# Performance work log

Hardware: AMD Instinct MI355X
Metric: run time of the kernel (lower is better)

## Reference

```python
import jax, jax.numpy as jnp
import numpy as np

D_MODEL = 1024
NUM_HEADS = 16
D_K = D_MODEL // NUM_HEADS


def setup_inputs() -> dict:
    key = jax.random.key(0)
    ks = jax.random.split(key, 9)
    B, S = 2, 2048
    scale = 1.0 / np.sqrt(D_MODEL)
    x = jax.random.normal(ks[0], (B, S, D_MODEL), dtype=jnp.float32)
    Wq = jax.random.normal(ks[1], (D_MODEL, D_MODEL), dtype=jnp.float32) * scale
    Wk = jax.random.normal(ks[2], (D_MODEL, D_MODEL), dtype=jnp.float32) * scale
    Wv = jax.random.normal(ks[3], (D_MODEL, D_MODEL), dtype=jnp.float32) * scale
    Wo = jax.random.normal(ks[4], (D_MODEL, D_MODEL), dtype=jnp.float32) * scale
    bq = jax.random.normal(ks[5], (D_MODEL,), dtype=jnp.float32) * 0.01
    bk = jax.random.normal(ks[6], (D_MODEL,), dtype=jnp.float32) * 0.01
    bv = jax.random.normal(ks[7], (D_MODEL,), dtype=jnp.float32) * 0.01
    bo = jax.random.normal(ks[8], (D_MODEL,), dtype=jnp.float32) * 0.01
    return {"x": x, "Wq": Wq, "bq": bq, "Wk": Wk, "bk": bk,
            "Wv": Wv, "bv": bv, "Wo": Wo, "bo": bo}


def reference(x, Wq, bq, Wk, bk, Wv, bv, Wo, bo):
    B, S, _ = x.shape
    H, Dk = NUM_HEADS, D_K
    # projections -> [B, H, S, Dk]
    def split_heads(t):
        return t.reshape(B, S, H, Dk).transpose(0, 2, 1, 3)
    q = split_heads(x @ Wq + bq)
    k = split_heads(x @ Wk + bk)
    v = split_heads(x @ Wv + bv)
    # full score matrix [B, H, S, S] (faithful to the original non-fused impl)
    scores = jnp.einsum('bhqd,bhkd->bhqk', q, k) / jnp.sqrt(jnp.float32(Dk))
    attn = jax.nn.softmax(scores, axis=-1)
    out = jnp.einsum('bhqk,bhkd->bhqd', attn, v)
    out = out.transpose(0, 2, 1, 3).reshape(B, S, H * Dk)
    return out @ Wo + bo
```

## Files before the change

### kernel.cpp

```cpp
#include <hip/hip_runtime.h>
#include <cstdint>

constexpr int S    = 2048;
constexpr int D    = 1024;
constexpr int NH   = 16;
constexpr int DK   = 64;
constexpr int MTOK = 2 * S;

typedef __bf16 bf16x8 __attribute__((ext_vector_type(8)));
typedef __bf16 bf16x4 __attribute__((ext_vector_type(4)));
typedef float  floatx4 __attribute__((ext_vector_type(4)));

__device__ __forceinline__ void async_cp16(const void* g, void* l) {
    __builtin_amdgcn_global_load_lds(
        (const __attribute__((address_space(1))) uint32_t*)g,
        (__attribute__((address_space(3))) uint32_t*)l, 16, 0, 0);
}

__global__ __launch_bounds__(256) void cvt_prep(
    const float* __restrict__ x, __bf16* __restrict__ xb,
    const float* __restrict__ W0, const float* __restrict__ W1,
    const float* __restrict__ W2, const float* __restrict__ W3,
    __bf16* __restrict__ T0, __bf16* __restrict__ T1,
    __bf16* __restrict__ T2, __bf16* __restrict__ T3)
{
    const int t = threadIdx.x;
    if (blockIdx.z == 4) {
        int blk = blockIdx.y * 16 + blockIdx.x;
        const float4* src = (const float4*)x;
        #pragma unroll
        for (int ii = 0; ii < 16; ++ii) {
            int idx = blk * 4096 + ii * 256 + t;
            float4 v = src[idx];
            bf16x4 o;
            o[0] = (__bf16)v.x; o[1] = (__bf16)v.y; o[2] = (__bf16)v.z; o[3] = (__bf16)v.w;
            *(bf16x4*)&xb[(size_t)idx * 4] = o;
        }
        return;
    }
    const float* W = (blockIdx.z == 0) ? W0 : (blockIdx.z == 1) ? W1 : (blockIdx.z == 2) ? W2 : W3;
    __bf16*      T = (blockIdx.z == 0) ? T0 : (blockIdx.z == 1) ? T1 : (blockIdx.z == 2) ? T2 : T3;
    __shared__ __bf16 tile[64][65];
    const int k0 = blockIdx.y * 64, n0 = blockIdx.x * 64;
    #pragma unroll
    for (int i = 0; i < 4; ++i) {
        int k = (t >> 4) + i * 16;
        int n = (t & 15) * 4;
        float4 v = *(const float4*)&W[(size_t)(k0 + k) * D + n0 + n];
        tile[n + 0][k] = (__bf16)v.x;
        tile[n + 1][k] = (__bf16)v.y;
        tile[n + 2][k] = (__bf16)v.z;
        tile[n + 3][k] = (__bf16)v.w;
    }
    __syncthreads();
    #pragma unroll
    for (int i = 0; i < 4; ++i) {
        int n = (t >> 4) + i * 16;
        int k = (t & 15) * 4;
        bf16x4 o;
        o[0] = tile[n][k]; o[1] = tile[n][k + 1]; o[2] = tile[n][k + 2]; o[3] = tile[n][k + 3];
        *(bf16x4*)&T[(size_t)(n0 + n) * D + k0 + k] = o;
    }
}

constexpr int BM = 128, BK = 64;

template<int JT>
__device__ __forceinline__ void gemm_core(
    const __bf16* __restrict__ A, const __bf16* __restrict__ Bt,
    __bf16* Alds, __bf16* Blds, int m0, int n0, floatx4 (&acc)[4][JT])
{
    const int tid = threadIdx.x;
    const int w = tid >> 6, l = tid & 63;
    const int wm = (w >> 1) * 64, wn = (w & 1) * 16 * JT;
    const int lr = l & 15, lg = l >> 4;

    #pragma unroll
    for (int i = 0; i < 4; ++i)
        #pragma unroll
        for (int j = 0; j < JT; ++j)
            acc[i][j] = (floatx4){0.f, 0.f, 0.f, 0.f};

    for (int k0 = 0; k0 < D; k0 += BK) {
        #pragma unroll
        for (int i = 0; i < 4; ++i) {
            int c = i * 256 + tid, row = c >> 3, g = c & 7;
            async_cp16(&A[(size_t)(m0 + row) * D + k0 + g * 8], &Alds[c * 8]);
        }
        #pragma unroll
        for (int i = 0; i < JT; ++i) {
            int c = i * 256 + tid, row = c >> 3, g = c & 7;
            async_cp16(&Bt[(size_t)(n0 + row) * D + k0 + g * 8], &Blds[c * 8]);
        }
        __syncthreads();
        #pragma unroll
        for (int kk = 0; kk < 2; ++kk) {
            bf16x8 af[4], bfr[JT];
            #pragma unroll
            for (int i = 0; i < 4; ++i)
                af[i] = *(const bf16x8*)&Alds[(wm + i * 16 + lr) * BK + kk * 32 + lg * 8];
            #pragma unroll
            for (int j = 0; j < JT; ++j)
                bfr[j] = *(const bf16x8*)&Blds[(wn + j * 16 + lr) * BK + kk * 32 + lg * 8];
            #pragma unroll
            for (int i = 0; i < 4; ++i)
                #pragma unroll
                for (int j = 0; j < JT; ++j)
                    acc[i][j] = __builtin_amdgcn_mfma_f32_16x16x32_bf16(af[i], bfr[j], acc[i][j], 0, 0, 0);
        }
        __syncthreads();
    }
}

__global__ __launch_bounds__(256, 2) void gemm_qkv(
    const __bf16* __restrict__ xb,
    const __bf16* __restrict__ WqT, const __bf16* __restrict__ WkT, const __bf16* __restrict__ WvT,
    const float* __restrict__ bq, const float* __restrict__ bk, const float* __restrict__ bv,
    __bf16* __restrict__ Qb, __bf16* __restrict__ Kb, __bf16* __restrict__ Vt)
{
    __shared__ __align__(16) __bf16 Alds[BM * BK];
    __shared__ __align__(16) __bf16 Blds[128 * BK];
    const int z = blockIdx.z;
    const __bf16* Bt   = (z == 0) ? WqT : (z == 1) ? WkT : WvT;
    const float*  bias = (z == 0) ? bq : (z == 1) ? bk : bv;
    const float   scale = (z == 0) ? 0.18033688f : 1.0f;
    const int m0 = blockIdx.y * BM, n0 = blockIdx.x * 128;

    floatx4 acc[4][4];
    gemm_core<4>(xb, Bt, Alds, Blds, m0, n0, acc);

    const int tid = threadIdx.x;
    const int w = tid >> 6, l = tid & 63;
    const int wm = (w >> 1) * 64, wn = (w & 1) * 64;
    const int lr = l & 15, lg = l >> 4;

    if (z < 2) {
        __bf16* Out = (z == 0) ? Qb : Kb;
        #pragma unroll
        for (int i = 0; i < 4; ++i)
            #pragma unroll
            for (int j = 0; j < 4; ++j) {
                int n = n0 + wn + j * 16 + lr;
                #pragma unroll
                for (int r = 0; r < 4; ++r) {
                    int m = m0 + wm + i * 16 + lg * 4 + r;
                    float v = (acc[i][j][r] + bias[n]) * scale;
                    size_t off = ((size_t)((m >> 11) * NH + (n >> 6)) * S + (m & (S - 1))) * DK + (n & (DK - 1));
                    Out[off] = (__bf16)v;
                }
            }
    } else {
        #pragma unroll
        for (int i = 0; i < 4; ++i)
            #pragma unroll
            for (int j = 0; j < 4; ++j) {
                int n = n0 + wn + j * 16 + lr;
                int m = m0 + wm + i * 16 + lg * 4;
                float bn = bias[n];
                bf16x4 o;
                #pragma unroll
                for (int r = 0; r < 4; ++r) o[r] = (__bf16)(acc[i][j][r] + bn);
                size_t off = ((size_t)((m >> 11) * NH + (n >> 6)) * DK + (n & (DK - 1))) * S + (m & (S - 1));
                *(bf16x4*)&Vt[off] = o;
            }
    }
}

__global__ __launch_bounds__(256, 2) void gemm_out(
    const __bf16* __restrict__ A, const __bf16* __restrict__ Bt,
    const float* __restrict__ bias, float* __restrict__ Cout)
{
    __shared__ __align__(16) __bf16 Alds[BM * BK];
    __shared__ __align__(16) __bf16 Blds[64 * BK];
    const int m0 = blockIdx.y * BM, n0 = blockIdx.x * 64;

    floatx4 acc[4][2];
    gemm_core<2>(A, Bt, Alds, Blds, m0, n0, acc);

    const int tid = threadIdx.x;
    const int w = tid >> 6, l = tid & 63;
    const int wm = (w >> 1) * 64, wn = (w & 1) * 32;
    const int lr = l & 15, lg = l >> 4;
    #pragma unroll
    for (int i = 0; i < 4; ++i)
        #pragma unroll
        for (int j = 0; j < 2; ++j) {
            int n = n0 + wn + j * 16 + lr;
            #pragma unroll
            for (int r = 0; r < 4; ++r) {
                int m = m0 + wm + i * 16 + lg * 4 + r;
                Cout[(size_t)m * D + n] = acc[i][j][r] + bias[n];
            }
        }
}

constexpr int QT = 128;
constexpr int KT = 64;
constexpr float SOFTMAX_C2 = 14.4269504f;

__global__ __launch_bounds__(256, 2) void attn_mfma(
    const __bf16* __restrict__ Q, const __bf16* __restrict__ K,
    const __bf16* __restrict__ Vt, __bf16* __restrict__ O)
{
    __shared__ __align__(16) __bf16 Klds[2][KT * DK];
    __shared__ __align__(16) __bf16 Vlds[2][DK * KT];
    __shared__ __align__(16) __bf16 Plds[4][32 * 64];

    const int tid = threadIdx.x;
    const int w = tid >> 6, l = tid & 63;
    const int lr = l & 15, lg = l >> 4;
    const int sw = lr & 7;
    const int bh = blockIdx.y;
    const int q0 = blockIdx.x * QT;
    const __bf16* Kbase = K  + (size_t)bh * S * DK;
    const __bf16* Vbase = Vt + (size_t)bh * DK * S;

    bf16x8 qf[2][2];
    {
        const __bf16* qp = Q + ((size_t)bh * S + q0 + w * 32) * DK;
        #pragma unroll
        for (int i = 0; i < 2; ++i)
            #pragma unroll
            for (int kk = 0; kk < 2; ++kk)
                qf[i][kk] = *(const bf16x8*)&qp[(i * 16 + lr) * DK + kk * 32 + lg * 8];
    }
    bf16x8 vones;
    #pragma unroll
    for (int j = 0; j < 8; ++j) vones[j] = (__bf16)1.0f;

    floatx4 acc[4][2];
    #pragma unroll
    for (int jd = 0; jd < 4; ++jd)
        #pragma unroll
        for (int i = 0; i < 2; ++i)
            acc[jd][i] = (floatx4){0.f, 0.f, 0.f, 0.f};
    floatx4 psacc[2];
    psacc[0] = (floatx4){0.f, 0.f, 0.f, 0.f};
    psacc[1] = (floatx4){0.f, 0.f, 0.f, 0.f};

    bf16x8 kreg[2], vreg[2];
    auto gload = [&](int t0) {
        #pragma unroll
        for (int ii = 0; ii < 2; ++ii) {
            int c = ii * 256 + tid, row = c >> 3, g = c & 7;
            kreg[ii] = *(const bf16x8*)&Kbase[(size_t)(t0 + row) * DK + g * 8];
            vreg[ii] = *(const bf16x8*)&Vbase[(size_t)row * S + t0 + g * 8];
        }
    };
    auto lwrite = [&](int buf) {
        #pragma unroll
        for (int ii = 0; ii < 2; ++ii) {
            int c = ii * 256 + tid, row = c >> 3, gs = (c & 7) ^ (row & 7);
            *(bf16x8*)&Klds[buf][row * 64 + gs * 8] = kreg[ii];
            *(bf16x8*)&Vlds[buf][row * 64 + gs * 8] = vreg[ii];
        }
    };

    gload(0);
    lwrite(0);
    gload(KT);

    for (int t0 = 0; t0 < S; t0 += KT) {
        const int cur = (t0 >> 6) & 1;
        __syncthreads();

        floatx4 sa[4][2];
        #pragma unroll
        for (int j = 0; j < 4; ++j)
            #pragma unroll
            for (int i = 0; i < 2; ++i)
                sa[j][i] = (floatx4){0.f, 0.f, 0.f, 0.f};
        #pragma unroll
        for (int kk = 0; kk < 2; ++kk) {
            bf16x8 kf[4];
            #pragma unroll
            for (int j = 0; j < 4; ++j)
                kf[j] = *(const bf16x8*)&Klds[cur][(j * 16 + lr) * DK + (((kk * 4 + lg) ^ sw) * 8)];
            #pragma unroll
            for (int j = 0; j < 4; ++j)
                #pragma unroll
                for (int i = 0; i < 2; ++i)
                    sa[j][i] = __builtin_amdgcn_mfma_f32_16x16x32_bf16(kf[j], qf[i][kk], sa[j][i], 0, 0, 0);
        }

        #pragma unroll
        for (int j = 0; j < 4; ++j)
            #pragma unroll
            for (int i = 0; i < 2; ++i) {
                bf16x4 pb;
                #pragma unroll
                for (int r = 0; r < 4; ++r)
                    pb[r] = (__bf16)__builtin_amdgcn_exp2f(sa[j][i][r] - SOFTMAX_C2);
                int gsw = (j * 2 + (lg >> 1)) ^ sw;
                *(bf16x4*)&Plds[w][(i * 16 + lr) * 64 + gsw * 8 + (lg & 1) * 4] = pb;
            }

        #pragma unroll
        for (int kk = 0; kk < 2; ++kk) {
            bf16x8 vf[4], pf[2];
            #pragma unroll
            for (int i = 0; i < 2; ++i) {
                int gsw = (kk * 4 + lg) ^ sw;
                pf[i] = *(const bf16x8*)&Plds[w][(i * 16 + lr) * 64 + gsw * 8];
            }
            #pragma unroll
            for (int jd = 0; jd < 4; ++jd)
                vf[jd] = *(const bf16x8*)&Vlds[cur][(jd * 16 + lr) * KT + (((kk * 4 + lg) ^ sw) * 8)];
            #pragma unroll
            for (int jd = 0; jd < 4; ++jd)
                #pragma unroll
                for (int i = 0; i < 2; ++i)
                    acc[jd][i] = __builtin_amdgcn_mfma_f32_16x16x32_bf16(vf[jd], pf[i], acc[jd][i], 0, 0, 0);
            #pragma unroll
            for (int i = 0; i < 2; ++i)
                psacc[i] = __builtin_amdgcn_mfma_f32_16x16x32_bf16(vones, pf[i], psacc[i], 0, 0, 0);
        }

        if (t0 + KT < S) {
            lwrite(cur ^ 1);
            if (t0 + 2 * KT < S) gload(t0 + 2 * KT);
        }
    }

    const int b = bh >> 4, h = bh & 15;
    #pragma unroll
    for (int i = 0; i < 2; ++i) {
        float inv = 1.f / psacc[i][0];
        int q = q0 + w * 32 + i * 16 + lr;
        __bf16* op = O + (size_t)(b * S + q) * D + h * DK;
        #pragma unroll
        for (int jd = 0; jd < 4; ++jd) {
            bf16x4 ov;
            #pragma unroll
            for (int r = 0; r < 4; ++r) ov[r] = (__bf16)(acc[jd][i][r] * inv);
            *(bf16x4*)&op[jd * 16 + lg * 4] = ov;
        }
    }
}

extern "C" void kernel_launch(void* const* d_in, const int* in_sizes, int n_in,
                              void* d_out, int out_size, void* d_ws, size_t ws_size,
                              hipStream_t stream) {
    const float* x  = (const float*)d_in[0];
    const float* Wq = (const float*)d_in[1];
    const float* bq = (const float*)d_in[2];
    const float* Wk = (const float*)d_in[3];
    const float* bk = (const float*)d_in[4];
    const float* Wv = (const float*)d_in[5];
    const float* bv = (const float*)d_in[6];
    const float* Wo = (const float*)d_in[7];
    const float* bo = (const float*)d_in[8];

    char* ws = (char*)d_ws;
    __bf16* xb  = (__bf16*)(ws);
    __bf16* WqT = (__bf16*)(ws + (8ull  << 20));
    __bf16* WkT = (__bf16*)(ws + (10ull << 20));
    __bf16* WvT = (__bf16*)(ws + (12ull << 20));
    __bf16* WoT = (__bf16*)(ws + (14ull << 20));
    __bf16* Qb  = (__bf16*)(ws + (16ull << 20));
    __bf16* Kb  = (__bf16*)(ws + (24ull << 20));
    __bf16* Vt  = (__bf16*)(ws + (32ull << 20));
    __bf16* Ob  = (__bf16*)(ws + (40ull << 20));

    cvt_prep<<<dim3(16, 16, 5), 256, 0, stream>>>(
        x, xb, Wq, Wk, Wv, Wo, WqT, WkT, WvT, WoT);

    gemm_qkv<<<dim3(D / 128, MTOK / BM, 3), 256, 0, stream>>>(
        xb, WqT, WkT, WvT, bq, bk, bv, Qb, Kb, Vt);

    attn_mfma<<<dim3(S / QT, 2 * NH), 256, 0, stream>>>(Qb, Kb, Vt, Ob);

    gemm_out<<<dim3(D / 64, MTOK / BM), 256, 0, stream>>>(Ob, WoT, bo, (float*)d_out);
}
```

Before: 194.2 us.

## Fuse Q/K/V projections into one GEMM sharing A tile, stage Q/K epilogue via LDS

The QKV projection kernel now computes all three projections in one block, loading each x tile into LDS once and reusing it against three 64-wide weight tiles, instead of launching a z-dimension of three separate GEMMs that each reloaded x. The Q and K epilogues are staged through a padded LDS tile so that each head row is written with 16-byte vector stores instead of scattered scalar bf16 stores. This cuts redundant global reads of x and uncoalesced writes. In exchange it uses more accumulator registers (three accumulator sets) and adds extra barriers, which may reduce occupancy.

```diff
diff --git a/kernel.cpp b/kernel.cpp
--- a/kernel.cpp
+++ b/kernel.cpp
@@ -118,51 +118,106 @@
     const float* __restrict__ bq, const float* __restrict__ bk, const float* __restrict__ bv,
     __bf16* __restrict__ Qb, __bf16* __restrict__ Kb, __bf16* __restrict__ Vt)
 {
-    __shared__ __align__(16) __bf16 Alds[BM * BK];
-    __shared__ __align__(16) __bf16 Blds[128 * BK];
-    const int z = blockIdx.z;
-    const __bf16* Bt   = (z == 0) ? WqT : (z == 1) ? WkT : WvT;
-    const float*  bias = (z == 0) ? bq : (z == 1) ? bk : bv;
-    const float   scale = (z == 0) ? 0.18033688f : 1.0f;
-    const int m0 = blockIdx.y * BM, n0 = blockIdx.x * 128;
-
-    floatx4 acc[4][4];
-    gemm_core<4>(xb, Bt, Alds, Blds, m0, n0, acc);
+    __shared__ __align__(16) char smem[40960];
+    __bf16* Alds = (__bf16*)smem;
+    __bf16* Blds = (__bf16*)(smem + 16384);
+    __bf16* Tep  = (__bf16*)smem;
 
     const int tid = threadIdx.x;
     const int w = tid >> 6, l = tid & 63;
-    const int wm = (w >> 1) * 64, wn = (w & 1) * 64;
+    const int wm = (w >> 1) * 64, wn = (w & 1) * 32;
     const int lr = l & 15, lg = l >> 4;
-
-    if (z < 2) {
+    const int m0 = blockIdx.y * BM, n0 = blockIdx.x * 64;
+
+    floatx4 acc[3][4][2];
+    #pragma unroll
+    for (int z = 0; z < 3; ++z)
+        #pragma unroll
+        for (int i = 0; i < 4; ++i)
+            #pragma unroll
+            for (int j = 0; j < 2; ++j)
+                acc[z][i][j] = (floatx4){0.f, 0.f, 0.f, 0.f};
+
+    const __bf16* Wz[3] = {WqT, WkT, WvT};
+
+    for (int k0 = 0; k0 < D; k0 += BK) {
+        #pragma unroll
+        for (int i = 0; i < 4; ++i) {
+            int c = i * 256 + tid, row = c >> 3, g = c & 7;
+            async_cp16(&xb[(size_t)(m0 + row) * D + k0 + g * 8], &Alds[c * 8]);
+        }
+        #pragma unroll
+        for (int z = 0; z < 3; ++z)
+            #pragma unroll
+            for (int i = 0; i < 2; ++i) {
+                int c = i * 256 + tid, row = c >> 3, g = c & 7;
+                async_cp16(&Wz[z][(size_t)(n0 + row) * D + k0 + g * 8],
+                           &Blds[(z * 4096) + c * 8]);
+            }
+        __syncthreads();
+        #pragma unroll
+        for (int kk = 0; kk < 2; ++kk) {
+            bf16x8 af[4];
+            #pragma unroll
+            for (int i = 0; i < 4; ++i)
+                af[i] = *(const bf16x8*)&Alds[(wm + i * 16 + lr) * BK + kk * 32 + lg * 8];
+            #pragma unroll
+            for (int z = 0; z < 3; ++z) {
+                bf16x8 bfr[2];
+                #pragma unroll
+                for (int j = 0; j < 2; ++j)
+                    bfr[j] = *(const bf16x8*)&Blds[z * 4096 + (wn + j * 16 + lr) * BK + kk * 32 + lg * 8];
+                #pragma unroll
+                for (int i = 0; i < 4; ++i)
+                    #pragma unroll
+                    for (int j = 0; j < 2; ++j)
+                        acc[z][i][j] = __builtin_amdgcn_mfma_f32_16x16x32_bf16(af[i], bfr[j], acc[z][i][j], 0, 0, 0);
+            }
+        }
+        __syncthreads();
+    }
+
+    const int b = m0 >> 11, h = n0 >> 6;
+    const int row = tid >> 1, half = tid & 1;
+
+    #pragma unroll
+    for (int i = 0; i < 4; ++i)
+        #pragma unroll
+        for (int j = 0; j < 2; ++j) {
+            int n = n0 + wn + j * 16 + lr;
+            int m = m0 + wm + i * 16 + lg * 4;
+            float bn = bv[n];
+            bf16x4 o;
+            #pragma unroll
+            for (int r = 0; r < 4; ++r) o[r] = (__bf16)(acc[2][i][j][r] + bn);
+            size_t off = ((size_t)(b * NH + h) * DK + (n & (DK - 1))) * S + (m & (S - 1));
+            *(bf16x4*)&Vt[off] = o;
+        }
+
+    #pragma unroll
+    for (int z = 0; z < 2; ++z) {
+        const float* bias = (z == 0) ? bq : bk;
+        const float scale = (z == 0) ? 0.18033688f : 1.0f;
         __bf16* Out = (z == 0) ? Qb : Kb;
+        __syncthreads();
         #pragma unroll
         for (int i = 0; i < 4; ++i)
             #pragma unroll
-            for (int j = 0; j < 4; ++j) {
-                int n = n0 + wn + j * 16 + lr;
+            for (int j = 0; j < 2; ++j) {
+                int nl = wn + j * 16 + lr;
+                float bn = bias[n0 + nl];
                 #pragma unroll
                 for (int r = 0; r < 4; ++r) {
-                    int m = m0 + wm + i * 16 + lg * 4 + r;
-                    float v = (acc[i][j][r] + bias[n]) * scale;
-                    size_t off = ((size_t)((m >> 11) * NH + (n >> 6)) * S + (m & (S - 1))) * DK + (n & (DK - 1));
-                    Out[off] = (__bf16)v;
+                    int ml = wm + i * 16 + lg * 4 + r;
+                    Tep[ml * 72 + nl] = (__bf16)((acc[z][i][j][r] + bn) * scale);
                 }
             }
-    } else {
-        #pragma unroll
-        for (int i = 0; i < 4; ++i)
-            #pragma unroll
-            for (int j = 0; j < 4; ++j) {
-                int n = n0 + wn + j * 16 + lr;
-                int m = m0 + wm + i * 16 + lg * 4;
-                float bn = bias[n];
-                bf16x4 o;
-                #pragma unroll
-                for (int r = 0; r < 4; ++r) o[r] = (__bf16)(acc[i][j][r] + bn);
-                size_t off = ((size_t)((m >> 11) * NH + (n >> 6)) * DK + (n & (DK - 1))) * S + (m & (S - 1));
-                *(bf16x4*)&Vt[off] = o;
-            }
+        __syncthreads();
+        int s_local = (m0 + row) & (S - 1);
+        __bf16* op = Out + ((size_t)(b * NH + h) * S + s_local) * DK + half * 32;
+        #pragma unroll
+        for (int c = 0; c < 4; ++c)
+            *(bf16x8*)&op[c * 8] = *(const bf16x8*)&Tep[row * 72 + half * 32 + c * 8];
     }
 }
 
@@ -365,7 +420,7 @@
     cvt_prep<<<dim3(16, 16, 5), 256, 0, stream>>>(
         x, xb, Wq, Wk, Wv, Wo, WqT, WkT, WvT, WoT);
 
-    gemm_qkv<<<dim3(D / 128, MTOK / BM, 3), 256, 0, stream>>>(
+    gemm_qkv<<<dim3(D / 64, MTOK / BM), 256, 0, stream>>>(
         xb, WqT, WkT, WvT, bq, bk, bv, Qb, Kb, Vt);
 
     attn_mfma<<<dim3(S / QT, 2 * NH), 256, 0, stream>>>(Qb, Kb, Vt, Ob);
```

New measurement: 194.7 us. No clear change (+0.3%).
